# Kernel tuning notes

Measured on AMD Instinct MI355X. Metric: run time of the kernel, lower is better.

Reference implementation:

```python
import jax, jax.numpy as jnp
import numpy as np

WS = 8          # window size
HEADS = 2
EPS = 1e-5      # torch LayerNorm default

def setup_inputs() -> dict:
    key = jax.random.key(0)
    ks = jax.random.split(key, 8)
    B, C, H, W = 4, 64, 512, 512
    hid = 128
    s = 0.02
    return {
        "x": jax.random.normal(ks[0], (B, C, H, W), jnp.float32),
        "norm1_g": jnp.ones((C,), jnp.float32),
        "norm1_b": jnp.zeros((C,), jnp.float32),
        "in_w": s * jax.random.normal(ks[1], (3 * C, C), jnp.float32),
        "in_b": jnp.zeros((3 * C,), jnp.float32),
        "out_w": s * jax.random.normal(ks[2], (C, C), jnp.float32),
        "out_b": jnp.zeros((C,), jnp.float32),
        "proj_w": s * jax.random.normal(ks[3], (C, C), jnp.float32),
        "proj_b": jnp.zeros((C,), jnp.float32),
        "norm2_g": jnp.ones((C,), jnp.float32),
        "norm2_b": jnp.zeros((C,), jnp.float32),
        "mlp_w1": s * jax.random.normal(ks[4], (hid, C), jnp.float32),
        "mlp_b1": jnp.zeros((hid,), jnp.float32),
        "mlp_w2": s * jax.random.normal(ks[5], (C, hid), jnp.float32),
        "mlp_b2": jnp.zeros((C,), jnp.float32),
    }

def _ln(t, g, b):
    m = jnp.mean(t, axis=-1, keepdims=True)
    v = jnp.mean(jnp.square(t - m), axis=-1, keepdims=True)
    return (t - m) * jax.lax.rsqrt(v + EPS) * g + b

def _block(x, norm1_g, norm1_b, in_w, in_b, out_w, out_b,
           proj_w, proj_b, norm2_g, norm2_b, mlp_w1, mlp_b1, mlp_w2, mlp_b2):
    B, C, H, W = x.shape
    ws = WS
    # H, W divisible by ws => pad_h = pad_w = 0 (module pads otherwise)
    # window partition: (B,C,H,W) -> (B*nWh*nWw, ws*ws, C)
    t = x.reshape(B, C, H // ws, ws, W // ws, ws)
    t = jnp.transpose(t, (0, 2, 4, 3, 5, 1))            # (B, nWh, nWw, ws, ws, C)
    tokens = t.reshape(-1, ws * ws, C)                  # (nw, T, C)
    nw, T, _ = tokens.shape
    dh = C // HEADS

    tn = _ln(tokens, norm1_g, norm1_b)
    # packed qkv projection (torch MultiheadAttention in_proj)
    qkv = tn @ in_w.T + in_b                            # (nw, T, 3C)
    q, k, v = jnp.split(qkv, 3, axis=-1)
    q = q.reshape(nw, T, HEADS, dh)
    k = k.reshape(nw, T, HEADS, dh)
    v = v.reshape(nw, T, HEADS, dh)
    scale = 1.0 / jnp.sqrt(jnp.asarray(dh, x.dtype))
    scores = jnp.einsum('nqhd,nkhd->nhqk', q, k) * scale  # (nw, H, T, T)
    attn = jax.nn.softmax(scores, axis=-1)
    o = jnp.einsum('nhqk,nkhd->nqhd', attn, v).reshape(nw, T, C)
    o = o @ out_w.T + out_b                             # MHA out_proj
    o = o @ proj_w.T + proj_b                           # extra proj
    tokens = tokens + o

    tn2 = _ln(tokens, norm2_g, norm2_b)
    h = jax.nn.gelu(tn2 @ mlp_w1.T + mlp_b1, approximate=False)
    tokens = tokens + (h @ mlp_w2.T + mlp_b2)

    # window reverse: (nw, T, C) -> (B, C, H, W)
    t = tokens.reshape(B, H // ws, W // ws, ws, ws, C)
    t = jnp.transpose(t, (0, 5, 1, 3, 2, 4))
    return t.reshape(B, C, H, W)

def reference(x, norm1_g, norm1_b, in_w, in_b, out_w, out_b,
              proj_w, proj_b, norm2_g, norm2_b, mlp_w1, mlp_b1, mlp_w2, mlp_b2):
    return _block(x, norm1_g, norm1_b, in_w, in_b, out_w, out_b,
                  proj_w, proj_b, norm2_g, norm2_b, mlp_w1, mlp_b1, mlp_w2, mlp_b2)
```

## Files before the change

kernel.cpp:

```cpp
#include <hip/hip_runtime.h>
#include <math.h>

#define HWs (512*512)

typedef short  s8v __attribute__((ext_vector_type(8)));
typedef float  f4v __attribute__((ext_vector_type(4)));

__device__ __forceinline__ float lo16(unsigned int u){ union{unsigned int i; float f;} z; z.i=u<<16;         return z.f; }
__device__ __forceinline__ float hi16(unsigned int u){ union{unsigned int i; float f;} z; z.i=u&0xffff0000u; return z.f; }
__device__ __forceinline__ unsigned int cvtpk(float lo, float hi){
  unsigned int r; asm("v_cvt_pk_bf16_f32 %0, %1, %2" : "=v"(r) : "v"(lo), "v"(hi)); return r;
}
__device__ __forceinline__ unsigned short f2bf(float f){ return (unsigned short)cvtpk(f,f); }
__device__ __forceinline__ unsigned short f2bf_rne(float f){
  union{float g; unsigned int u;} a; a.g=f;
  unsigned int r = a.u + 0x7fffu + ((a.u>>16)&1u);
  return (unsigned short)(r>>16);
}

#define SWZ(row) (((((row)&7) ^ (((row)>>3)&7)))<<4)

__global__ void conv_wb(const float* __restrict__ inw, const float* __restrict__ w1,
                        const float* __restrict__ w2, unsigned short* __restrict__ ws){
  int i = blockIdx.x*256 + threadIdx.x;
  if (i < 12288)      ws[i] = f2bf_rne(inw[i]);
  else if (i < 20480) ws[i] = f2bf_rne(w1[i-12288]);
  else                ws[i] = f2bf_rne(w2[i-20480]);
}

__global__ void fuse_proj_kernel(const float* __restrict__ out_w, const float* __restrict__ out_b,
                                 const float* __restrict__ proj_w, const float* __restrict__ proj_b,
                                 unsigned short* __restrict__ wf_bf, float* __restrict__ bfv){
  int i = blockIdx.x*256 + threadIdx.x;
  if (i >= 64*64) return;
  int c = i>>6, k = i&63;
  float acc = 0.f;
  for (int m=0;m<64;m++) acc += proj_w[c*64+m]*out_w[m*64+k];
  wf_bf[i] = f2bf_rne(acc);
  if (k==0){
    float ab = proj_b[c];
    for (int m=0;m<64;m++) ab += proj_w[c*64+m]*out_b[m];
    bfv[c] = ab;
  }
}

__global__ __launch_bounds__(1024,4) void hat_main(
    const float* __restrict__ x,
    const float* __restrict__ n1g, const float* __restrict__ n1b,
    const float* __restrict__ inb,
    const unsigned short* __restrict__ wbf,
    const float* __restrict__ bfv,
    const float* __restrict__ n2g, const float* __restrict__ n2b,
    const float* __restrict__ b1, const float* __restrict__ b2,
    float* __restrict__ out)
{
  __shared__ __align__(16) unsigned char lds[131072];
  #define RA 0
  #define RB 8192
  #define RC 16384
  #define RD 24576

  const int t = threadIdx.x;
  const int l = t & 63;
  const int g = (l>>4)&3, c = l&15;
  const int w = t>>6;
  const int tm = w>>2;
  const int wb = (w&3)<<15;
  const int cb = t>>8;
  const int pr = (t>>5)&7;
  const int pc = t&31;
  const int tok = pr*8 + (pc&7);
  const int wtb = ((pc>>3)&3)<<15;

  const int n = blockIdx.x;
  const int ww4 = n&15, wh=(n>>4)&63, b=n>>10;
  const size_t pix = (size_t)(wh*8+pr)*512 + ww4*32 + pc;
  const float* xp = x + ((size_t)b*64 + 16*cb)*HWs + pix;

  const unsigned short* inw_bf = wbf;
  const unsigned short* w1_bf  = wbf + 12288;
  const unsigned short* w2_bf  = wbf + 20480;
  const unsigned short* wf_bf  = wbf + 28672;

  float xr[16];
  #pragma unroll
  for (int i=0;i<16;i++) xr[i] = xp[(size_t)i*HWs];
  {
    float s1=0.f, s2=0.f;
    #pragma unroll
    for (int i=0;i<16;i++){ s1 += xr[i]; s2 += xr[i]*xr[i]; }
    *(float2*)(lds + wtb + RD + tok*32 + cb*8) = make_float2(s1, s2);
  }
  __syncthreads();

  unsigned int xres[8];
  {
    float S=0.f, SS=0.f;
    #pragma unroll
    for (int grp=0; grp<4; grp++){
      float2 p = *(const float2*)(lds + wtb + RD + tok*32 + grp*8);
      S += p.x; SS += p.y;
    }
    float mu = S*(1.f/64.f);
    float var = SS*(1.f/64.f) - mu*mu;
    float rstd = rsqrtf(var + 1e-5f);
    float tv[16];
    #pragma unroll
    for (int i=0;i<16;i++) tv[i] = (xr[i]-mu)*rstd*n1g[16*cb+i] + n1b[16*cb+i];
    #pragma unroll
    for (int j=0;j<8;j++) xres[j] = cvtpk(xr[2*j], xr[2*j+1]);
    uint4 W0, W1;
    W0.x=cvtpk(tv[0],tv[1]);  W0.y=cvtpk(tv[2],tv[3]);  W0.z=cvtpk(tv[4],tv[5]);  W0.w=cvtpk(tv[6],tv[7]);
    W1.x=cvtpk(tv[8],tv[9]);  W1.y=cvtpk(tv[10],tv[11]);W1.z=cvtpk(tv[12],tv[13]);W1.w=cvtpk(tv[14],tv[15]);
    int sw = SWZ(tok);
    *(uint4*)(lds + wtb + RA + tok*128 + ((32*cb   ) ^ sw)) = W0;
    *(uint4*)(lds + wtb + RA + tok*128 + ((32*cb+16) ^ sw)) = W1;
  }
  __syncthreads();

  const int row_a = 16*tm + c;
  const int swa = SWZ(row_a);
  const float scale = 0.17677669529663688f;

  {
    s8v a0 = *(const s8v*)(lds + wb + RA + row_a*128 + ((16*g   ) ^ swa));
    s8v a1 = *(const s8v*)(lds + wb + RA + row_a*128 + ((64+16*g) ^ swa));
    #pragma unroll 1
    for (int chunk=0; chunk<2; chunk++){
      f4v acc[4] = {};
      #pragma unroll
      for (int tn=0;tn<4;tn++){
        s8v bf0 = *(const s8v*)(inw_bf + (64*chunk+16*tn+c)*64 + 8*g);
        s8v bf1 = *(const s8v*)(inw_bf + (64*chunk+16*tn+c)*64 + 32 + 8*g);
        acc[tn] = __builtin_amdgcn_mfma_f32_16x16x32_bf16(a0, bf0, acc[tn], 0,0,0);
        acc[tn] = __builtin_amdgcn_mfma_f32_16x16x32_bf16(a1, bf1, acc[tn], 0,0,0);
      }
      const int reg = (chunk==0) ? RB : RC;
      #pragma unroll
      for (int tn=0;tn<4;tn++){
        float bias = inb[64*chunk + 16*tn + c];
        #pragma unroll
        for (int r=0;r<4;r++){
          float v = acc[tn][r] + bias;
          if (chunk==0) v *= scale;
          int row = 16*tm + 4*g + r;
          *(unsigned short*)(lds + wb + reg + row*128 + ((2*(16*tn+c)) ^ SWZ(row))) = f2bf(v);
        }
      }
    }
    {
      f4v acc[4] = {};
      #pragma unroll
      for (int tn=0;tn<4;tn++){
        s8v bf0 = *(const s8v*)(inw_bf + (128+16*tn+c)*64 + 8*g);
        s8v bf1 = *(const s8v*)(inw_bf + (128+16*tn+c)*64 + 32 + 8*g);
        acc[tn] = __builtin_amdgcn_mfma_f32_16x16x32_bf16(a0, bf0, acc[tn], 0,0,0);
        acc[tn] = __builtin_amdgcn_mfma_f32_16x16x32_bf16(a1, bf1, acc[tn], 0,0,0);
      }
      #pragma unroll
      for (int tn=0;tn<4;tn++){
        int drow = 16*tn + c;
        float bias = inb[128 + drow];
        uint2 U;
        U.x = cvtpk(acc[tn][0]+bias, acc[tn][1]+bias);
        U.y = cvtpk(acc[tn][2]+bias, acc[tn][3]+bias);
        *(uint2*)(lds + wb + RD + drow*128 + ((2*(16*tm+4*g)) ^ SWZ(drow))) = U;
      }
    }
  }
  __syncthreads();

  f4v oacc[4] = {};
  #pragma unroll 1
  for (int h=0; h<2; h++){
    s8v qa = *(const s8v*)(lds + wb + RB + row_a*128 + ((64*h+16*g) ^ swa));
    f4v sacc[4] = {};
    #pragma unroll
    for (int tn=0;tn<4;tn++){
      int kr = 16*tn + c;
      s8v kb = *(const s8v*)(lds + wb + RC + kr*128 + ((64*h+16*g) ^ SWZ(kr)));
      sacc[tn] = __builtin_amdgcn_mfma_f32_16x16x32_bf16(qa, kb, sacc[tn], 0,0,0);
    }
    float mrow[4], lr[4];
    #pragma unroll
    for (int r=0;r<4;r++)
      mrow[r] = fmaxf(fmaxf(sacc[0][r],sacc[1][r]), fmaxf(sacc[2][r],sacc[3][r]));
    #pragma unroll
    for (int mk=1; mk<16; mk<<=1)
      #pragma unroll
      for (int r=0;r<4;r++) mrow[r] = fmaxf(mrow[r], __shfl_xor(mrow[r], mk));
    #pragma unroll
    for (int r=0;r<4;r++){
      float s0 = 0.f;
      #pragma unroll
      for (int tn=0;tn<4;tn++){
        float p = __expf(sacc[tn][r] - mrow[r]);
        sacc[tn][r] = p; s0 += p;
      }
      lr[r] = s0;
    }
    #pragma unroll
    for (int mk=1; mk<16; mk<<=1)
      #pragma unroll
      for (int r=0;r<4;r++) lr[r] += __shfl_xor(lr[r], mk);
    #pragma unroll
    for (int r=0;r<4;r++){
      float inv = 1.f/lr[r];
      int row = 16*tm + 4*g + r;
      int sw = SWZ(row);
      #pragma unroll
      for (int tn=0;tn<4;tn++)
        *(unsigned short*)(lds + wb + RA + row*128 + ((2*(16*tn+c)) ^ sw)) = f2bf(sacc[tn][r]*inv);
    }
    s8v pa0 = *(const s8v*)(lds + wb + RA + row_a*128 + ((16*g   ) ^ swa));
    s8v pa1 = *(const s8v*)(lds + wb + RA + row_a*128 + ((64+16*g) ^ swa));
    #pragma unroll
    for (int tnl=0; tnl<2; tnl++){
      int vr = 32*h + 16*tnl + c;
      int svr = SWZ(vr);
      s8v vb0 = *(const s8v*)(lds + wb + RD + vr*128 + ((16*g   ) ^ svr));
      s8v vb1 = *(const s8v*)(lds + wb + RD + vr*128 + ((64+16*g) ^ svr));
      oacc[2*h+tnl] = __builtin_amdgcn_mfma_f32_16x16x32_bf16(pa0, vb0, oacc[2*h+tnl], 0,0,0);
      oacc[2*h+tnl] = __builtin_amdgcn_mfma_f32_16x16x32_bf16(pa1, vb1, oacc[2*h+tnl], 0,0,0);
    }
  }
  #pragma unroll
  for (int r=0;r<4;r++){
    int row = 16*tm + 4*g + r;
    int sw = SWZ(row);
    #pragma unroll
    for (int j=0;j<4;j++)
      *(unsigned short*)(lds + wb + RB + row*128 + ((2*(16*j+c)) ^ sw)) = f2bf(oacc[j][r]);
  }
  __syncthreads();

  {
    s8v oa0 = *(const s8v*)(lds + wb + RB + row_a*128 + ((16*g   ) ^ swa));
    s8v oa1 = *(const s8v*)(lds + wb + RB + row_a*128 + ((64+16*g) ^ swa));
    f4v acc[4] = {};
    #pragma unroll
    for (int tn=0;tn<4;tn++){
      s8v bf0 = *(const s8v*)(wf_bf + (16*tn+c)*64 + 8*g);
      s8v bf1 = *(const s8v*)(wf_bf + (16*tn+c)*64 + 32 + 8*g);
      acc[tn] = __builtin_amdgcn_mfma_f32_16x16x32_bf16(oa0, bf0, acc[tn], 0,0,0);
      acc[tn] = __builtin_amdgcn_mfma_f32_16x16x32_bf16(oa1, bf1, acc[tn], 0,0,0);
    }
    #pragma unroll
    for (int tn=0;tn<4;tn++){
      float bias = bfv[16*tn+c];
      #pragma unroll
      for (int r=0;r<4;r++){
        int row = 16*tm + 4*g + r;
        *(unsigned short*)(lds + wb + RC + row*128 + ((2*(16*tn+c)) ^ SWZ(row))) = f2bf(acc[tn][r] + bias);
      }
    }
  }
  __syncthreads();

  float row2[16];
  {
    int sw = SWZ(tok);
    uint4 A0 = *(const uint4*)(lds + wtb + RC + tok*128 + ((32*cb   ) ^ sw));
    uint4 A1 = *(const uint4*)(lds + wtb + RC + tok*128 + ((32*cb+16) ^ sw));
    unsigned int pr8[8] = {A0.x,A0.y,A0.z,A0.w,A1.x,A1.y,A1.z,A1.w};
    #pragma unroll
    for (int j=0;j<8;j++){
      row2[2*j]   = lo16(pr8[j]) + lo16(xres[j]);
      row2[2*j+1] = hi16(pr8[j]) + hi16(xres[j]);
    }
    float s1=0.f, s2=0.f;
    #pragma unroll
    for (int i=0;i<16;i++){ s1 += row2[i]; s2 += row2[i]*row2[i]; }
    *(float2*)(lds + wtb + RB + tok*32 + cb*8) = make_float2(s1, s2);
  }
  __syncthreads();
  {
    float S=0.f, SS=0.f;
    #pragma unroll
    for (int grp=0; grp<4; grp++){
      float2 p = *(const float2*)(lds + wtb + RB + tok*32 + grp*8);
      S += p.x; SS += p.y;
    }
    float mu2 = S*(1.f/64.f);
    float v2 = SS*(1.f/64.f) - mu2*mu2;
    float rstd2 = rsqrtf(v2 + 1e-5f);
    float tv[16];
    #pragma unroll
    for (int i=0;i<16;i++) tv[i] = (row2[i]-mu2)*rstd2*n2g[16*cb+i] + n2b[16*cb+i];
    uint4 W0, W1;
    W0.x=cvtpk(tv[0],tv[1]);  W0.y=cvtpk(tv[2],tv[3]);  W0.z=cvtpk(tv[4],tv[5]);  W0.w=cvtpk(tv[6],tv[7]);
    W1.x=cvtpk(tv[8],tv[9]);  W1.y=cvtpk(tv[10],tv[11]);W1.z=cvtpk(tv[12],tv[13]);W1.w=cvtpk(tv[14],tv[15]);
    int sw = SWZ(tok);
    *(uint4*)(lds + wtb + RA + tok*128 + ((32*cb   ) ^ sw)) = W0;
    *(uint4*)(lds + wtb + RA + tok*128 + ((32*cb+16) ^ sw)) = W1;
  }
  __syncthreads();

  {
    s8v la0 = *(const s8v*)(lds + wb + RA + row_a*128 + ((16*g   ) ^ swa));
    s8v la1 = *(const s8v*)(lds + wb + RA + row_a*128 + ((64+16*g) ^ swa));
    #pragma unroll 1
    for (int nch=0; nch<2; nch++){
      f4v acc[4] = {};
      #pragma unroll
      for (int tn=0;tn<4;tn++){
        s8v bf0 = *(const s8v*)(w1_bf + (64*nch+16*tn+c)*64 + 8*g);
        s8v bf1 = *(const s8v*)(w1_bf + (64*nch+16*tn+c)*64 + 32 + 8*g);
        acc[tn] = __builtin_amdgcn_mfma_f32_16x16x32_bf16(la0, bf0, acc[tn], 0,0,0);
        acc[tn] = __builtin_amdgcn_mfma_f32_16x16x32_bf16(la1, bf1, acc[tn], 0,0,0);
      }
      const int reg = nch ? RD : RB;
      #pragma unroll
      for (int tn=0;tn<4;tn++){
        float bias = b1[64*nch + 16*tn + c];
        #pragma unroll
        for (int r=0;r<4;r++){
          float v = acc[tn][r] + bias;
          float z = v*(1.595769122f + 0.071354816f*v*v);
          float sg = 1.f/(1.f + __expf(-z));
          int row = 16*tm + 4*g + r;
          *(unsigned short*)(lds + wb + reg + row*128 + ((2*(16*tn+c)) ^ SWZ(row))) = f2bf(v*sg);
        }
      }
    }
  }
  {
    f4v acc[4] = {};
    #pragma unroll
    for (int kk=0;kk<4;kk++){
      const int reg = (kk<2) ? RB : RD;
      s8v ha = *(const s8v*)(lds + wb + reg + row_a*128 + ((64*(kk&1)+16*g) ^ swa));
      #pragma unroll
      for (int tn=0;tn<4;tn++){
        s8v bf = *(const s8v*)(w2_bf + (16*tn+c)*128 + 32*kk + 8*g);
        acc[tn] = __builtin_amdgcn_mfma_f32_16x16x32_bf16(ha, bf, acc[tn], 0,0,0);
      }
    }
    #pragma unroll
    for (int tn=0;tn<4;tn++){
      float bias = b2[16*tn+c];
      #pragma unroll
      for (int r=0;r<4;r++){
        int row = 16*tm + 4*g + r;
        *(unsigned short*)(lds + wb + RA + row*128 + ((2*(16*tn+c)) ^ SWZ(row))) = f2bf(acc[tn][r] + bias);
      }
    }
  }
  __syncthreads();

  {
    int sw = SWZ(tok);
    uint4 A0 = *(const uint4*)(lds + wtb + RA + tok*128 + ((32*cb   ) ^ sw));
    uint4 A1 = *(const uint4*)(lds + wtb + RA + tok*128 + ((32*cb+16) ^ sw));
    unsigned int pr8[8] = {A0.x,A0.y,A0.z,A0.w,A1.x,A1.y,A1.z,A1.w};
    float* op = out + ((size_t)b*64 + 16*cb)*HWs + pix;
    #pragma unroll
    for (int j=0;j<8;j++){
      op[(size_t)(2*j  )*HWs] = lo16(pr8[j]) + row2[2*j];
      op[(size_t)(2*j+1)*HWs] = hi16(pr8[j]) + row2[2*j+1];
    }
  }
}

extern "C" void kernel_launch(void* const* d_in, const int* in_sizes, int n_in,
                              void* d_out, int out_size, void* d_ws, size_t ws_size,
                              hipStream_t stream) {
  const float* x    = (const float*)d_in[0];
  const float* n1g  = (const float*)d_in[1];
  const float* n1b  = (const float*)d_in[2];
  const float* inw  = (const float*)d_in[3];
  const float* inb  = (const float*)d_in[4];
  const float* outw = (const float*)d_in[5];
  const float* outb = (const float*)d_in[6];
  const float* pw   = (const float*)d_in[7];
  const float* pb   = (const float*)d_in[8];
  const float* n2g  = (const float*)d_in[9];
  const float* n2b  = (const float*)d_in[10];
  const float* w1   = (const float*)d_in[11];
  const float* b1   = (const float*)d_in[12];
  const float* w2   = (const float*)d_in[13];
  const float* b2   = (const float*)d_in[14];

  unsigned short* wsu = (unsigned short*)d_ws;
  unsigned short* wf_bf = wsu + 28672;
  float* bfv = (float*)((char*)d_ws + 65536);

  hipLaunchKernelGGL(conv_wb, dim3(112), dim3(256), 0, stream, inw, w1, w2, wsu);
  hipLaunchKernelGGL(fuse_proj_kernel, dim3(16), dim3(256), 0, stream, outw, outb, pw, pb, wf_bf, bfv);
  hipLaunchKernelGGL(hat_main, dim3(4096), dim3(1024), 0, stream,
                     x, n1g, n1b, inb, wsu, bfv, n2g, n2b, b1, b2, (float*)d_out);
}
```

Baseline: 769.3 us.

## Transpose MFMA operands for vectorized LDS stores and halve block size

```diff
diff --git a/kernel.cpp b/kernel.cpp
--- a/kernel.cpp
+++ b/kernel.cpp
@@ -4,6 +4,7 @@
 #define HWs (512*512)
 
 typedef short  s8v __attribute__((ext_vector_type(8)));
+typedef short  s4v __attribute__((ext_vector_type(4)));
 typedef float  f4v __attribute__((ext_vector_type(4)));
 
 __device__ __forceinline__ float lo16(unsigned int u){ union{unsigned int i; float f;} z; z.i=u<<16;         return z.f; }
@@ -11,11 +12,18 @@
 __device__ __forceinline__ unsigned int cvtpk(float lo, float hi){
   unsigned int r; asm("v_cvt_pk_bf16_f32 %0, %1, %2" : "=v"(r) : "v"(lo), "v"(hi)); return r;
 }
-__device__ __forceinline__ unsigned short f2bf(float f){ return (unsigned short)cvtpk(f,f); }
 __device__ __forceinline__ unsigned short f2bf_rne(float f){
   union{float g; unsigned int u;} a; a.g=f;
   unsigned int r = a.u + 0x7fffu + ((a.u>>16)&1u);
   return (unsigned short)(r>>16);
+}
+__device__ __forceinline__ void st8(void* p, unsigned int a, unsigned int b){
+  union{ unsigned int u[2]; s4v v; } z; z.u[0]=a; z.u[1]=b;
+  *(s4v*)p = z.v;
+}
+__device__ __forceinline__ void st16(void* p, unsigned int a, unsigned int b, unsigned int c, unsigned int d){
+  union{ unsigned int u[4]; s8v v; } z; z.u[0]=a; z.u[1]=b; z.u[2]=c; z.u[3]=d;
+  *(s8v*)p = z.v;
 }
 
 #define SWZ(row) (((((row)&7) ^ (((row)>>3)&7)))<<4)
@@ -44,7 +52,7 @@
   }
 }
 
-__global__ __launch_bounds__(1024,4) void hat_main(
+__global__ __launch_bounds__(512,4) void hat_main(
     const float* __restrict__ x,
     const float* __restrict__ n1g, const float* __restrict__ n1b,
     const float* __restrict__ inb,
@@ -54,7 +62,7 @@
     const float* __restrict__ b1, const float* __restrict__ b2,
     float* __restrict__ out)
 {
-  __shared__ __align__(16) unsigned char lds[131072];
+  __shared__ __align__(16) unsigned char lds[65536];
   #define RA 0
   #define RB 8192
   #define RC 16384
@@ -63,18 +71,18 @@
   const int t = threadIdx.x;
   const int l = t & 63;
   const int g = (l>>4)&3, c = l&15;
-  const int w = t>>6;
-  const int tm = w>>2;
-  const int wb = (w&3)<<15;
-  const int cb = t>>8;
-  const int pr = (t>>5)&7;
-  const int pc = t&31;
+  const int w  = t>>6;
+  const int tm = w>>1;
+  const int wb = (w&1)<<15;
+  const int cb = t>>7;
+  const int pr = (t>>4)&7;
+  const int pc = t&15;
   const int tok = pr*8 + (pc&7);
-  const int wtb = ((pc>>3)&3)<<15;
+  const int wtb = ((pc>>3)&1)<<15;
 
   const int n = blockIdx.x;
-  const int ww4 = n&15, wh=(n>>4)&63, b=n>>10;
-  const size_t pix = (size_t)(wh*8+pr)*512 + ww4*32 + pc;
+  const int ww2 = n&31, wh=(n>>5)&63, b=n>>11;
+  const size_t pix = (size_t)(wh*8+pr)*512 + ww2*16 + pc;
   const float* xp = x + ((size_t)b*64 + 16*cb)*HWs + pix;
 
   const unsigned short* inw_bf = wbf;
@@ -109,12 +117,11 @@
     for (int i=0;i<16;i++) tv[i] = (xr[i]-mu)*rstd*n1g[16*cb+i] + n1b[16*cb+i];
     #pragma unroll
     for (int j=0;j<8;j++) xres[j] = cvtpk(xr[2*j], xr[2*j+1]);
-    uint4 W0, W1;
-    W0.x=cvtpk(tv[0],tv[1]);  W0.y=cvtpk(tv[2],tv[3]);  W0.z=cvtpk(tv[4],tv[5]);  W0.w=cvtpk(tv[6],tv[7]);
-    W1.x=cvtpk(tv[8],tv[9]);  W1.y=cvtpk(tv[10],tv[11]);W1.z=cvtpk(tv[12],tv[13]);W1.w=cvtpk(tv[14],tv[15]);
     int sw = SWZ(tok);
-    *(uint4*)(lds + wtb + RA + tok*128 + ((32*cb   ) ^ sw)) = W0;
-    *(uint4*)(lds + wtb + RA + tok*128 + ((32*cb+16) ^ sw)) = W1;
+    st16(lds + wtb + RA + tok*128 + ((32*cb   ) ^ sw),
+         cvtpk(tv[0],tv[1]), cvtpk(tv[2],tv[3]), cvtpk(tv[4],tv[5]), cvtpk(tv[6],tv[7]));
+    st16(lds + wtb + RA + tok*128 + ((32*cb+16) ^ sw),
+         cvtpk(tv[8],tv[9]), cvtpk(tv[10],tv[11]), cvtpk(tv[12],tv[13]), cvtpk(tv[14],tv[15]));
   }
   __syncthreads();
 
@@ -122,55 +129,46 @@
   const int swa = SWZ(row_a);
   const float scale = 0.17677669529663688f;
 
-  {
-    s8v a0 = *(const s8v*)(lds + wb + RA + row_a*128 + ((16*g   ) ^ swa));
-    s8v a1 = *(const s8v*)(lds + wb + RA + row_a*128 + ((64+16*g) ^ swa));
-    #pragma unroll 1
-    for (int chunk=0; chunk<2; chunk++){
-      f4v acc[4] = {};
-      #pragma unroll
-      for (int tn=0;tn<4;tn++){
-        s8v bf0 = *(const s8v*)(inw_bf + (64*chunk+16*tn+c)*64 + 8*g);
-        s8v bf1 = *(const s8v*)(inw_bf + (64*chunk+16*tn+c)*64 + 32 + 8*g);
-        acc[tn] = __builtin_amdgcn_mfma_f32_16x16x32_bf16(a0, bf0, acc[tn], 0,0,0);
-        acc[tn] = __builtin_amdgcn_mfma_f32_16x16x32_bf16(a1, bf1, acc[tn], 0,0,0);
-      }
-      const int reg = (chunk==0) ? RB : RC;
-      #pragma unroll
-      for (int tn=0;tn<4;tn++){
-        float bias = inb[64*chunk + 16*tn + c];
-        #pragma unroll
-        for (int r=0;r<4;r++){
-          float v = acc[tn][r] + bias;
-          if (chunk==0) v *= scale;
-          int row = 16*tm + 4*g + r;
-          *(unsigned short*)(lds + wb + reg + row*128 + ((2*(16*tn+c)) ^ SWZ(row))) = f2bf(v);
-        }
-      }
-    }
-    {
-      f4v acc[4] = {};
-      #pragma unroll
-      for (int tn=0;tn<4;tn++){
-        s8v bf0 = *(const s8v*)(inw_bf + (128+16*tn+c)*64 + 8*g);
-        s8v bf1 = *(const s8v*)(inw_bf + (128+16*tn+c)*64 + 32 + 8*g);
-        acc[tn] = __builtin_amdgcn_mfma_f32_16x16x32_bf16(a0, bf0, acc[tn], 0,0,0);
-        acc[tn] = __builtin_amdgcn_mfma_f32_16x16x32_bf16(a1, bf1, acc[tn], 0,0,0);
-      }
-      #pragma unroll
-      for (int tn=0;tn<4;tn++){
-        int drow = 16*tn + c;
-        float bias = inb[128 + drow];
-        uint2 U;
-        U.x = cvtpk(acc[tn][0]+bias, acc[tn][1]+bias);
-        U.y = cvtpk(acc[tn][2]+bias, acc[tn][3]+bias);
-        *(uint2*)(lds + wb + RD + drow*128 + ((2*(16*tm+4*g)) ^ SWZ(drow))) = U;
-      }
-    }
-  }
-  __syncthreads();
-
-  f4v oacc[4] = {};
+  s8v a0 = *(const s8v*)(lds + wb + RA + row_a*128 + ((16*g   ) ^ swa));
+  s8v a1 = *(const s8v*)(lds + wb + RA + row_a*128 + ((64+16*g) ^ swa));
+  #pragma unroll 1
+  for (int chunk=0; chunk<2; chunk++){
+    f4v acc[4] = {};
+    #pragma unroll
+    for (int tn=0;tn<4;tn++){
+      s8v wf0 = *(const s8v*)(inw_bf + (64*chunk+16*tn+c)*64 + 8*g);
+      s8v wf1 = *(const s8v*)(inw_bf + (64*chunk+16*tn+c)*64 + 32 + 8*g);
+      acc[tn] = __builtin_amdgcn_mfma_f32_16x16x32_bf16(wf0, a0, acc[tn], 0,0,0);
+      acc[tn] = __builtin_amdgcn_mfma_f32_16x16x32_bf16(wf1, a1, acc[tn], 0,0,0);
+    }
+    const int reg = (chunk==0) ? RB : RC;
+    #pragma unroll
+    for (int tn=0;tn<4;tn++){
+      float4 b4 = *(const float4*)(inb + 64*chunk + 16*tn + 4*g);
+      float v0=acc[tn][0]+b4.x, v1=acc[tn][1]+b4.y, v2=acc[tn][2]+b4.z, v3=acc[tn][3]+b4.w;
+      if (chunk==0){ v0*=scale; v1*=scale; v2*=scale; v3*=scale; }
+      st8(lds + wb + reg + row_a*128 + ((2*(16*tn+4*g)) ^ swa), cvtpk(v0,v1), cvtpk(v2,v3));
+    }
+  }
+  {
+    f4v acc[4] = {};
+    #pragma unroll
+    for (int tn=0;tn<4;tn++){
+      s8v wf0 = *(const s8v*)(inw_bf + (128+16*tn+c)*64 + 8*g);
+      s8v wf1 = *(const s8v*)(inw_bf + (128+16*tn+c)*64 + 32 + 8*g);
+      acc[tn] = __builtin_amdgcn_mfma_f32_16x16x32_bf16(a0, wf0, acc[tn], 0,0,0);
+      acc[tn] = __builtin_amdgcn_mfma_f32_16x16x32_bf16(a1, wf1, acc[tn], 0,0,0);
+    }
+    #pragma unroll
+    for (int tn=0;tn<4;tn++){
+      int drow = 16*tn + c;
+      float bias = inb[128 + drow];
+      st8(lds + wb + RD + drow*128 + ((2*(16*tm+4*g)) ^ SWZ(drow)),
+          cvtpk(acc[tn][0]+bias, acc[tn][1]+bias), cvtpk(acc[tn][2]+bias, acc[tn][3]+bias));
+    }
+  }
+  __syncthreads();
+
   #pragma unroll 1
   for (int h=0; h<2; h++){
     s8v qa = *(const s8v*)(lds + wb + RB + row_a*128 + ((64*h+16*g) ^ swa));
@@ -179,39 +177,29 @@
     for (int tn=0;tn<4;tn++){
       int kr = 16*tn + c;
       s8v kb = *(const s8v*)(lds + wb + RC + kr*128 + ((64*h+16*g) ^ SWZ(kr)));
-      sacc[tn] = __builtin_amdgcn_mfma_f32_16x16x32_bf16(qa, kb, sacc[tn], 0,0,0);
-    }
-    float mrow[4], lr[4];
-    #pragma unroll
-    for (int r=0;r<4;r++)
-      mrow[r] = fmaxf(fmaxf(sacc[0][r],sacc[1][r]), fmaxf(sacc[2][r],sacc[3][r]));
-    #pragma unroll
-    for (int mk=1; mk<16; mk<<=1)
+      sacc[tn] = __builtin_amdgcn_mfma_f32_16x16x32_bf16(kb, qa, sacc[tn], 0,0,0);
+    }
+    float mt[4];
+    #pragma unroll
+    for (int tn=0;tn<4;tn++)
+      mt[tn] = fmaxf(fmaxf(sacc[tn][0],sacc[tn][1]), fmaxf(sacc[tn][2],sacc[tn][3]));
+    float m = fmaxf(fmaxf(mt[0],mt[1]), fmaxf(mt[2],mt[3]));
+    m = fmaxf(m, __shfl_xor(m, 16));
+    m = fmaxf(m, __shfl_xor(m, 32));
+    float lsum = 0.f;
+    float p[4][4];
+    #pragma unroll
+    for (int tn=0;tn<4;tn++)
       #pragma unroll
-      for (int r=0;r<4;r++) mrow[r] = fmaxf(mrow[r], __shfl_xor(mrow[r], mk));
-    #pragma unroll
-    for (int r=0;r<4;r++){
-      float s0 = 0.f;
-      #pragma unroll
-      for (int tn=0;tn<4;tn++){
-        float p = __expf(sacc[tn][r] - mrow[r]);
-        sacc[tn][r] = p; s0 += p;
-      }
-      lr[r] = s0;
-    }
-    #pragma unroll
-    for (int mk=1; mk<16; mk<<=1)
-      #pragma unroll
-      for (int r=0;r<4;r++) lr[r] += __shfl_xor(lr[r], mk);
-    #pragma unroll
-    for (int r=0;r<4;r++){
-      float inv = 1.f/lr[r];
-      int row = 16*tm + 4*g + r;
-      int sw = SWZ(row);
-      #pragma unroll
-      for (int tn=0;tn<4;tn++)
-        *(unsigned short*)(lds + wb + RA + row*128 + ((2*(16*tn+c)) ^ sw)) = f2bf(sacc[tn][r]*inv);
-    }
+      for (int r=0;r<4;r++){ float e = __expf(sacc[tn][r]-m); p[tn][r]=e; lsum+=e; }
+    lsum += __shfl_xor(lsum, 16);
+    lsum += __shfl_xor(lsum, 32);
+    float inv = 1.f/lsum;
+    #pragma unroll
+    for (int tn=0;tn<4;tn++)
+      st8(lds + wb + RA + row_a*128 + ((2*(16*tn+4*g)) ^ swa),
+          cvtpk(p[tn][0]*inv, p[tn][1]*inv), cvtpk(p[tn][2]*inv, p[tn][3]*inv));
+    asm volatile("" ::: "memory");
     s8v pa0 = *(const s8v*)(lds + wb + RA + row_a*128 + ((16*g   ) ^ swa));
     s8v pa1 = *(const s8v*)(lds + wb + RA + row_a*128 + ((64+16*g) ^ swa));
     #pragma unroll
@@ -220,17 +208,12 @@
       int svr = SWZ(vr);
       s8v vb0 = *(const s8v*)(lds + wb + RD + vr*128 + ((16*g   ) ^ svr));
       s8v vb1 = *(const s8v*)(lds + wb + RD + vr*128 + ((64+16*g) ^ svr));
-      oacc[2*h+tnl] = __builtin_amdgcn_mfma_f32_16x16x32_bf16(pa0, vb0, oacc[2*h+tnl], 0,0,0);
-      oacc[2*h+tnl] = __builtin_amdgcn_mfma_f32_16x16x32_bf16(pa1, vb1, oacc[2*h+tnl], 0,0,0);
-    }
-  }
-  #pragma unroll
-  for (int r=0;r<4;r++){
-    int row = 16*tm + 4*g + r;
-    int sw = SWZ(row);
-    #pragma unroll
-    for (int j=0;j<4;j++)
-      *(unsigned short*)(lds + wb + RB + row*128 + ((2*(16*j+c)) ^ sw)) = f2bf(oacc[j][r]);
+      f4v oc = {};
+      oc = __builtin_amdgcn_mfma_f32_16x16x32_bf16(vb0, pa0, oc, 0,0,0);
+      oc = __builtin_amdgcn_mfma_f32_16x16x32_bf16(vb1, pa1, oc, 0,0,0);
+      st8(lds + wb + RB + row_a*128 + ((64*h + 32*tnl + 8*g) ^ swa),
+          cvtpk(oc[0], oc[1]), cvtpk(oc[2], oc[3]));
+    }
   }
   __syncthreads();
 
@@ -240,19 +223,16 @@
     f4v acc[4] = {};
     #pragma unroll
     for (int tn=0;tn<4;tn++){
-      s8v bf0 = *(const s8v*)(wf_bf + (16*tn+c)*64 + 8*g);
-      s8v bf1 = *(const s8v*)(wf_bf + (16*tn+c)*64 + 32 + 8*g);
-      acc[tn] = __builtin_amdgcn_mfma_f32_16x16x32_bf16(oa0, bf0, acc[tn], 0,0,0);
-      acc[tn] = __builtin_amdgcn_mfma_f32_16x16x32_bf16(oa1, bf1, acc[tn], 0,0,0);
-    }
-    #pragma unroll
-    for (int tn=0;tn<4;tn++){
-      float bias = bfv[16*tn+c];
-      #pragma unroll
-      for (int r=0;r<4;r++){
-        int row = 16*tm + 4*g + r;
-        *(unsigned short*)(lds + wb + RC + row*128 + ((2*(16*tn+c)) ^ SWZ(row))) = f2bf(acc[tn][r] + bias);
-      }
+      s8v wf0 = *(const s8v*)(wf_bf + (16*tn+c)*64 + 8*g);
+      s8v wf1 = *(const s8v*)(wf_bf + (16*tn+c)*64 + 32 + 8*g);
+      acc[tn] = __builtin_amdgcn_mfma_f32_16x16x32_bf16(wf0, oa0, acc[tn], 0,0,0);
+      acc[tn] = __builtin_amdgcn_mfma_f32_16x16x32_bf16(wf1, oa1, acc[tn], 0,0,0);
+    }
+    #pragma unroll
+    for (int tn=0;tn<4;tn++){
+      float4 b4 = *(const float4*)(bfv + 16*tn + 4*g);
+      st8(lds + wb + RC + row_a*128 + ((2*(16*tn+4*g)) ^ swa),
+          cvtpk(acc[tn][0]+b4.x, acc[tn][1]+b4.y), cvtpk(acc[tn][2]+b4.z, acc[tn][3]+b4.w));
     }
   }
   __syncthreads();
@@ -287,12 +267,11 @@
     float tv[16];
     #pragma unroll
     for (int i=0;i<16;i++) tv[i] = (row2[i]-mu2)*rstd2*n2g[16*cb+i] + n2b[16*cb+i];
-    uint4 W0, W1;
-    W0.x=cvtpk(tv[0],tv[1]);  W0.y=cvtpk(tv[2],tv[3]);  W0.z=cvtpk(tv[4],tv[5]);  W0.w=cvtpk(tv[6],tv[7]);
-    W1.x=cvtpk(tv[8],tv[9]);  W1.y=cvtpk(tv[10],tv[11]);W1.z=cvtpk(tv[12],tv[13]);W1.w=cvtpk(tv[14],tv[15]);
     int sw = SWZ(tok);
-    *(uint4*)(lds + wtb + RA + tok*128 + ((32*cb   ) ^ sw)) = W0;
-    *(uint4*)(lds + wtb + RA + tok*128 + ((32*cb+16) ^ sw)) = W1;
+    st16(lds + wtb + RA + tok*128 + ((32*cb   ) ^ sw),
+         cvtpk(tv[0],tv[1]), cvtpk(tv[2],tv[3]), cvtpk(tv[4],tv[5]), cvtpk(tv[6],tv[7]));
+    st16(lds + wtb + RA + tok*128 + ((32*cb+16) ^ sw),
+         cvtpk(tv[8],tv[9]), cvtpk(tv[10],tv[11]), cvtpk(tv[12],tv[13]), cvtpk(tv[14],tv[15]));
   }
   __syncthreads();
 
@@ -304,26 +283,27 @@
       f4v acc[4] = {};
       #pragma unroll
       for (int tn=0;tn<4;tn++){
-        s8v bf0 = *(const s8v*)(w1_bf + (64*nch+16*tn+c)*64 + 8*g);
-        s8v bf1 = *(const s8v*)(w1_bf + (64*nch+16*tn+c)*64 + 32 + 8*g);
-        acc[tn] = __builtin_amdgcn_mfma_f32_16x16x32_bf16(la0, bf0, acc[tn], 0,0,0);
-        acc[tn] = __builtin_amdgcn_mfma_f32_16x16x32_bf16(la1, bf1, acc[tn], 0,0,0);
+        s8v wf0 = *(const s8v*)(w1_bf + (64*nch+16*tn+c)*64 + 8*g);
+        s8v wf1 = *(const s8v*)(w1_bf + (64*nch+16*tn+c)*64 + 32 + 8*g);
+        acc[tn] = __builtin_amdgcn_mfma_f32_16x16x32_bf16(wf0, la0, acc[tn], 0,0,0);
+        acc[tn] = __builtin_amdgcn_mfma_f32_16x16x32_bf16(wf1, la1, acc[tn], 0,0,0);
       }
       const int reg = nch ? RD : RB;
       #pragma unroll
       for (int tn=0;tn<4;tn++){
-        float bias = b1[64*nch + 16*tn + c];
+        float4 b4 = *(const float4*)(b1 + 64*nch + 16*tn + 4*g);
+        float vv[4] = {acc[tn][0]+b4.x, acc[tn][1]+b4.y, acc[tn][2]+b4.z, acc[tn][3]+b4.w};
         #pragma unroll
         for (int r=0;r<4;r++){
-          float v = acc[tn][r] + bias;
+          float v = vv[r];
           float z = v*(1.595769122f + 0.071354816f*v*v);
-          float sg = 1.f/(1.f + __expf(-z));
-          int row = 16*tm + 4*g + r;
-          *(unsigned short*)(lds + wb + reg + row*128 + ((2*(16*tn+c)) ^ SWZ(row))) = f2bf(v*sg);
+          vv[r] = v/(1.f + __expf(-z));
         }
+        st8(lds + wb + reg + row_a*128 + ((2*(16*tn+4*g)) ^ swa), cvtpk(vv[0],vv[1]), cvtpk(vv[2],vv[3]));
       }
     }
   }
+  asm volatile("" ::: "memory");
   {
     f4v acc[4] = {};
     #pragma unroll
@@ -332,18 +312,15 @@
       s8v ha = *(const s8v*)(lds + wb + reg + row_a*128 + ((64*(kk&1)+16*g) ^ swa));
       #pragma unroll
       for (int tn=0;tn<4;tn++){
-        s8v bf = *(const s8v*)(w2_bf + (16*tn+c)*128 + 32*kk + 8*g);
-        acc[tn] = __builtin_amdgcn_mfma_f32_16x16x32_bf16(ha, bf, acc[tn], 0,0,0);
+        s8v wf = *(const s8v*)(w2_bf + (16*tn+c)*128 + 32*kk + 8*g);
+        acc[tn] = __builtin_amdgcn_mfma_f32_16x16x32_bf16(wf, ha, acc[tn], 0,0,0);
       }
     }
     #pragma unroll
     for (int tn=0;tn<4;tn++){
-      float bias = b2[16*tn+c];
-      #pragma unroll
-      for (int r=0;r<4;r++){
-        int row = 16*tm + 4*g + r;
-        *(unsigned short*)(lds + wb + RA + row*128 + ((2*(16*tn+c)) ^ SWZ(row))) = f2bf(acc[tn][r] + bias);
-      }
+      float4 b4 = *(const float4*)(b2 + 16*tn + 4*g);
+      st8(lds + wb + RA + row_a*128 + ((2*(16*tn+4*g)) ^ swa),
+          cvtpk(acc[tn][0]+b4.x, acc[tn][1]+b4.y), cvtpk(acc[tn][2]+b4.z, acc[tn][3]+b4.w));
     }
   }
   __syncthreads();
@@ -387,6 +364,6 @@
 
   hipLaunchKernelGGL(conv_wb, dim3(112), dim3(256), 0, stream, inw, w1, w2, wsu);
   hipLaunchKernelGGL(fuse_proj_kernel, dim3(16), dim3(256), 0, stream, outw, outb, pw, pb, wf_bf, bfv);
-  hipLaunchKernelGGL(hat_main, dim3(4096), dim3(1024), 0, stream,
+  hipLaunchKernelGGL(hat_main, dim3(8192), dim3(512), 0, stream,
                      x, n1g, n1b, inb, wsu, bfv, n2g, n2b, b1, b2, (float*)d_out);
 }
```

New measurement: 648.8 us. -15.7%, faster.
